# Kernel optimization log

Measured on AMD Instinct MI355X. Metric: run time of the kernel, lower is better.

## Reference

```python
import jax, jax.numpy as jnp
import numpy as np

def setup_inputs() -> dict:
    key = jax.random.key(0)
    k1, k2, k3, k4 = jax.random.split(key, 4)
    B, T, C, H = 4, 4096, 1024, 64
    x = jax.random.normal(k1, (B, T, C), dtype=jnp.float32)
    Wk = jax.random.normal(k2, (C, H), dtype=jnp.float32) * (C ** -0.5)
    Wq = jax.random.normal(k3, (C, H), dtype=jnp.float32) * (C ** -0.5)
    Wv = jax.random.normal(k4, (C, H), dtype=jnp.float32) * (C ** -0.5)
    return {"x": x, "Wk": Wk, "Wq": Wq, "Wv": Wv}

def reference(x, Wk, Wq, Wv):
    B, T, C = x.shape
    k = x @ Wk          # [B,T,H]
    q = x @ Wq          # [B,T,H]
    v = x @ Wv          # [B,T,H]
    # NOTE: original scales by C**-0.5 (full embed dim), not head_size**-0.5
    scale = C ** -0.5
    wei = jnp.einsum('bqh,bkh->bqk', q, k) * scale          # [B,T,T]
    causal = jnp.tril(jnp.ones((T, T), dtype=bool))
    wei = jnp.where(causal, wei, -jnp.inf)
    wei = jax.nn.softmax(wei, axis=-1)
    # dropout is identity in eval mode
    out = jnp.einsum('bqk,bkh->bqh', wei, v)                # [B,T,H]
    return out
```

## Files before the change

kernel.cpp:

```cpp
#include <hip/hip_runtime.h>
#include <hip/hip_bf16.h>
#include <stdint.h>

#define T_SEQ 4096
#define CDIM 1024
#define HDIM 64
#define M0 4.0f

typedef __attribute__((ext_vector_type(8))) short short8;
typedef __attribute__((ext_vector_type(4))) short short4v;
typedef __attribute__((ext_vector_type(8))) __bf16 bf16x8;
typedef __attribute__((ext_vector_type(4))) float f32x4;

static __device__ __forceinline__ short f2bf(float f) {
    uint32_t u = __builtin_bit_cast(uint32_t, f);
    u += 0x7FFFu + ((u >> 16) & 1u);
    return (short)(u >> 16);
}

static __device__ __forceinline__ f32x4 mfma16(short8 a, short8 b, f32x4 c) {
    return __builtin_amdgcn_mfma_f32_16x16x32_bf16(
        __builtin_bit_cast(bf16x8, a), __builtin_bit_cast(bf16x8, b), c, 0, 0, 0);
}

static __device__ __forceinline__ void gload_lds16(const void* g, void* l) {
    __builtin_amdgcn_global_load_lds(
        (const __attribute__((address_space(1))) void*)g,
        (__attribute__((address_space(3))) void*)l, 16, 0, 0);
}

__global__ void prep_w2(const float* __restrict__ Wk, const float* __restrict__ Wq,
                        const float* __restrict__ Wv, short* __restrict__ W2) {
    const int d = blockIdx.x * 256 + threadIdx.x;
    const int j = d & 7, l = (d >> 3) & 63;
    const int f = d >> 9;
    const int nt2 = f % 12, rest = f / 12;
    const int i = rest & 15, s = rest >> 4;
    const int n = s * 96 + (nt2 >> 1) * 16 + (l & 15);
    const int k = i * 64 + (nt2 & 1) * 32 + ((l >> 4) << 3) + j;
    float v;
    if (n < 64)       v = Wq[k * 64 + n] * (0.03125f * 1.44269504088896340736f);
    else if (n < 128) v = Wk[k * 64 + (n - 64)];
    else              v = Wv[k * 64 + (n - 128)];
    W2[d] = f2bf(v);
}

__global__ __launch_bounds__(256) void proj(const float* __restrict__ x,
                                            const short* __restrict__ W2,
                                            short* __restrict__ Qo,
                                            short* __restrict__ Ko,
                                            short* __restrict__ VT) {
    __shared__ __align__(16) short tX[2][2048];
    const int tid = threadIdx.x;
    const int lane = tid & 63, wave = tid >> 6;
    const int r = lane & 15, g = lane >> 4;
    const int msub = wave >> 1, nsplit = wave & 1;
    const int m0 = blockIdx.x * 32;

    const int srow = tid >> 3, sc = tid & 7;
    const float* xgp = x + (size_t)(m0 + srow) * CDIM + sc * 8;
    short* xd = &tX[0][srow * 64 + ((sc ^ (srow & 7)) << 3)];
    const int bufstride = 2048;

    const int arow = msub * 16 + r;
    const int aoff0 = arow * 64 + (((0 + g) ^ (arow & 7)) << 3);
    const int aoff1 = arow * 64 + (((4 + g) ^ (arow & 7)) << 3);

    const short* w2base = W2 + (size_t)nsplit * 16 * 6144 + lane * 8;

    f32x4 acc[6];
    #pragma unroll
    for (int i = 0; i < 6; ++i) acc[i] = (f32x4){0.f, 0.f, 0.f, 0.f};

    short8 wA[12], wB[12];
    {
        const short* wp = w2base;
        #pragma unroll
        for (int f = 0; f < 12; ++f) wA[f] = *(const short8*)(wp + f * 512);
    }

    f32x4 a0 = *(const f32x4*)(xgp);
    f32x4 a1 = *(const f32x4*)(xgp + 4);
    {
        short8 v;
        #pragma unroll
        for (int q = 0; q < 4; ++q) { v[q] = f2bf(a0[q]); v[4 + q] = f2bf(a1[q]); }
        *(short8*)xd = v;
    }
    a0 = *(const f32x4*)(xgp + 64);
    a1 = *(const f32x4*)(xgp + 64 + 4);
    __syncthreads();

    auto step = [&](int i, short8 (&WC)[12], short8 (&WN)[12]) {
        if (i + 1 < 16) {
            const short* wp = w2base + (size_t)(i + 1) * 6144;
            #pragma unroll
            for (int f = 0; f < 12; ++f) WN[f] = *(const short8*)(wp + f * 512);
        }
        if (i + 1 < 16) {
            short8 v;
            #pragma unroll
            for (int q = 0; q < 4; ++q) { v[q] = f2bf(a0[q]); v[4 + q] = f2bf(a1[q]); }
            *(short8*)(xd + ((i & 1) ? 0 : bufstride)) = v;
        }
        if (i + 2 < 16) {
            a0 = *(const f32x4*)(xgp + (i + 2) * 64);
            a1 = *(const f32x4*)(xgp + (i + 2) * 64 + 4);
        }
        const short* Xt = &tX[i & 1][0];
        short8 xf0 = *(const short8*)(Xt + aoff0);
        short8 xf1 = *(const short8*)(Xt + aoff1);
        #pragma unroll
        for (int nt = 0; nt < 6; ++nt) {
            if (nsplit == 1 && nt >= 2) {
                acc[nt] = mfma16(WC[2 * nt], xf0, acc[nt]);
                acc[nt] = mfma16(WC[2 * nt + 1], xf1, acc[nt]);
            } else {
                acc[nt] = mfma16(xf0, WC[2 * nt], acc[nt]);
                acc[nt] = mfma16(xf1, WC[2 * nt + 1], acc[nt]);
            }
        }
        __syncthreads();
    };

    for (int ii = 0; ii < 16; ii += 2) {
        step(ii, wA, wB);
        step(ii + 1, wB, wA);
    }

    const int b = m0 >> 12;
    const int tb = m0 & (T_SEQ - 1);
    if (nsplit == 0) {
        #pragma unroll
        for (int nt = 0; nt < 4; ++nt)
            #pragma unroll
            for (int rr = 0; rr < 4; ++rr)
                Qo[(size_t)(m0 + msub * 16 + g * 4 + rr) * HDIM + nt * 16 + r] = f2bf(acc[nt][rr]);
        #pragma unroll
        for (int nt = 4; nt < 6; ++nt)
            #pragma unroll
            for (int rr = 0; rr < 4; ++rr)
                Ko[(size_t)(m0 + msub * 16 + g * 4 + rr) * HDIM + (nt - 4) * 16 + r] = f2bf(acc[nt][rr]);
    } else {
        #pragma unroll
        for (int nt = 0; nt < 2; ++nt)
            #pragma unroll
            for (int rr = 0; rr < 4; ++rr)
                Ko[(size_t)(m0 + msub * 16 + g * 4 + rr) * HDIM + 32 + nt * 16 + r] = f2bf(acc[nt][rr]);
        const int kpanel = tb >> 6;
        const int kk0 = (tb & 63) + msub * 16;
        #pragma unroll
        for (int nt = 2; nt < 6; ++nt)
            #pragma unroll
            for (int rr = 0; rr < 4; ++rr) {
                const int h = (nt - 2) * 16 + g * 4 + rr;
                VT[(((size_t)b * 64 + kpanel) * 64 + h) * 64 + kk0 + r] = f2bf(acc[nt][rr]);
            }
    }
}

__global__ __launch_bounds__(256) void attn(const short* __restrict__ Q,
                                            const short* __restrict__ K,
                                            const short* __restrict__ VT,
                                            float* __restrict__ out,
                                            float* __restrict__ opart,
                                            float* __restrict__ lpart) {
    __shared__ __align__(16) short tK[2][4096];
    __shared__ __align__(16) short tV[2][4096];

    const int tid = threadIdx.x;
    const int lane = tid & 63, wave = tid >> 6;
    const int r = lane & 15, g = lane >> 4;
    const int b = blockIdx.x & 3;
    const int s = (int)(blockIdx.x >> 2) & 3;
    const int u = (int)(blockIdx.x >> 4);
    const int quad = u >> 4, v5 = u & 15;
    int qt;
    if (quad == 0)      qt = 63 - v5;
    else if (quad == 1) qt = v5;
    else if (quad == 2) qt = 47 - v5;
    else                qt = 16 + v5;
    const int qs = qt * 64 + wave * 16;
    const int n64 = qt + 1;
    const int niters = (n64 > s) ? ((n64 - s + 3) >> 2) : 0;

    const short* Qb = Q + (size_t)b * T_SEQ * HDIM;
    const short* Kb = K + (size_t)b * T_SEQ * HDIM;
    const short* Vb = VT + (size_t)b * 64 * 64 * 64;

    short8 qf0 = *(const short8*)(Qb + (qs + r) * HDIM + g * 8);
    short8 qf1 = *(const short8*)(Qb + (qs + r) * HDIM + 32 + g * 8);

    const int lrow = lane >> 3;
    const int lchk = (lane & 7) ^ lrow;
    const short* kgp0 = Kb + (size_t)(s * 64 + wave * 16 + lrow) * 64 + lchk * 8;
    const short* kgp1 = Kb + (size_t)(s * 64 + wave * 16 + 8 + lrow) * 64 + lchk * 8;
    const short* vgp0 = Vb + (size_t)s * 4096 + (wave * 16 + lrow) * 64 + lchk * 8;
    const short* vgp1 = Vb + (size_t)s * 4096 + (wave * 16 + 8 + lrow) * 64 + lchk * 8;
    const int ldso0 = (wave * 2) * 512, ldso1 = (wave * 2 + 1) * 512;

    int kfo0[4], kfo1[4];
    #pragma unroll
    for (int kk = 0; kk < 4; ++kk) {
        kfo0[kk] = (kk * 16 + r) * 64 + (((0 + g) ^ (r & 7)) << 3);
        kfo1[kk] = (kk * 16 + r) * 64 + (((4 + g) ^ (r & 7)) << 3);
    }
    int voL[2][4], voH[2][4];
    #pragma unroll
    for (int w2 = 0; w2 < 2; ++w2)
        #pragma unroll
        for (int ht = 0; ht < 4; ++ht) {
            const int h = ht * 16 + r;
            voL[w2][ht] = h * 64 + (((w2 * 4 + (g >> 1)) ^ (r & 7)) << 3) + (g & 1) * 4;
            voH[w2][ht] = h * 64 + (((w2 * 4 + 2 + (g >> 1)) ^ (r & 7)) << 3) + (g & 1) * 4;
        }

    float lrun = 0.f;
    f32x4 o[4];
    #pragma unroll
    for (int i = 0; i < 4; ++i) o[i] = (f32x4){0.f, 0.f, 0.f, 0.f};
    const int tq = qs + r;

    if (niters > 0) {
        gload_lds16(kgp0, &tK[0][ldso0]);
        gload_lds16(kgp1, &tK[0][ldso1]);
        gload_lds16(vgp0, &tV[0][ldso0]);
        gload_lds16(vgp1, &tV[0][ldso1]);
        __syncthreads();

        for (int i = 0; i < niters; ++i) {
            if (i + 1 < niters) {
                const int bn = (i + 1) & 1;
                const size_t adv = (size_t)(i + 1) * 16384;
                gload_lds16(kgp0 + adv, &tK[bn][ldso0]);
                gload_lds16(kgp1 + adv, &tK[bn][ldso1]);
                gload_lds16(vgp0 + adv, &tV[bn][ldso0]);
                gload_lds16(vgp1 + adv, &tV[bn][ldso1]);
            }
            const int ktm = (4 * i + s) * 64;
            const short* Kt = &tK[i & 1][0];
            const short* Vt = &tV[i & 1][0];

            short8 pf[2];
            __builtin_amdgcn_s_setprio(1);
            #pragma unroll
            for (int kk = 0; kk < 4; ++kk) {
                short8 kf0 = *(const short8*)(Kt + kfo0[kk]);
                short8 kf1 = *(const short8*)(Kt + kfo1[kk]);
                f32x4 sv4 = mfma16(kf0, qf0, (f32x4){0.f, 0.f, 0.f, 0.f});
                sv4 = mfma16(kf1, qf1, sv4);
                #pragma unroll
                for (int rr = 0; rr < 4; ++rr) {
                    const int kg = ktm + kk * 16 + g * 4 + rr;
                    float sv = sv4[rr];
                    sv = (kg <= tq) ? sv : -1e30f;
                    const float pv = __builtin_amdgcn_exp2f(sv - M0);
                    lrun += pv;
                    pf[kk >> 1][(kk & 1) * 4 + rr] = f2bf(pv);
                }
            }
            #pragma unroll
            for (int ht = 0; ht < 4; ++ht) {
                #pragma unroll
                for (int w2 = 0; w2 < 2; ++w2) {
                    short4v lo = *(const short4v*)(Vt + voL[w2][ht]);
                    short4v hi = *(const short4v*)(Vt + voH[w2][ht]);
                    short8 vf;
                    #pragma unroll
                    for (int q4 = 0; q4 < 4; ++q4) { vf[q4] = lo[q4]; vf[4 + q4] = hi[q4]; }
                    o[ht] = mfma16(vf, pf[w2], o[ht]);
                }
            }
            __builtin_amdgcn_s_setprio(0);
            __syncthreads();
        }
    }

    lrun += __shfl_xor(lrun, 16);
    lrun += __shfl_xor(lrun, 32);
    const int row = (b << 12) + qs + r;
    if (g == 0) lpart[s * 16384 + row] = lrun;
    float* ob = (s == 0 ? out : opart + (size_t)(s - 1) * 16384 * HDIM) + (size_t)row * HDIM;
    #pragma unroll
    for (int ht = 0; ht < 4; ++ht)
        *(f32x4*)(ob + ht * 16 + g * 4) = o[ht];
}

__global__ __launch_bounds__(256) void norm4(float* __restrict__ out,
                                             const float* __restrict__ opart,
                                             const float* __restrict__ lpart) {
    const int i4 = blockIdx.x * 256 + threadIdx.x;
    const int row = i4 >> 4;
    f32x4 v = *(const f32x4*)(out + (size_t)i4 * 4);
    #pragma unroll
    for (int s = 0; s < 3; ++s)
        v += *(const f32x4*)(opart + (size_t)s * 16384 * HDIM + (size_t)i4 * 4);
    const float inv = 1.0f / (lpart[row] + lpart[16384 + row] +
                              lpart[2 * 16384 + row] + lpart[3 * 16384 + row]);
    v *= inv;
    *(f32x4*)(out + (size_t)i4 * 4) = v;
}

extern "C" void kernel_launch(void* const* d_in, const int* in_sizes, int n_in,
                              void* d_out, int out_size, void* d_ws, size_t ws_size,
                              hipStream_t stream) {
    const float* x  = (const float*)d_in[0];
    const float* Wk = (const float*)d_in[1];
    const float* Wq = (const float*)d_in[2];
    const float* Wv = (const float*)d_in[3];
    float* out = (float*)d_out;

    char* ws = (char*)d_ws;
    short* W2 = (short*)ws;
    short* Qb = (short*)(ws + 393216);
    short* Kb = (short*)(ws + 393216 + 2097152);
    short* VT = (short*)(ws + 393216 + 2 * 2097152);
    float* opart = (float*)(ws + 393216 + 3 * 2097152);
    float* lpart = (float*)(ws + 393216 + 3 * 2097152 + 3 * 4194304);

    prep_w2<<<768, 256, 0, stream>>>(Wk, Wq, Wv, W2);
    proj<<<512, 256, 0, stream>>>(x, W2, Qb, Kb, VT);
    attn<<<1024, 256, 0, stream>>>(Qb, Kb, VT, out, opart, lpart);
    norm4<<<1024, 256, 0, stream>>>(out, opart, lpart);
}
```

Measured before the change: 56.58 us.

## Split each attention key tile across two waves per query sub-block

Doubles the attention block to 512 threads (8 waves). Each pair of waves shares one 16-row query slice, and each wave of the pair handles half of the 64-key tile. The two partial outputs and row sums are combined through shared memory at the end. This cuts the per-wave serial MFMA/exp chain per iteration in half and spreads the tile loads over more waves, which should improve latency hiding. The cost is an extra LDS reduction, a block-wide barrier, and more threads per block competing for occupancy.

```diff
diff --git a/kernel.cpp b/kernel.cpp
--- a/kernel.cpp
+++ b/kernel.cpp
@@ -159,18 +159,18 @@
     }
 }
 
-__global__ __launch_bounds__(256) void attn(const short* __restrict__ Q,
-                                            const short* __restrict__ K,
-                                            const short* __restrict__ VT,
-                                            float* __restrict__ out,
-                                            float* __restrict__ opart,
-                                            float* __restrict__ lpart) {
-    __shared__ __align__(16) short tK[2][4096];
-    __shared__ __align__(16) short tV[2][4096];
+__global__ __launch_bounds__(512, 8) void attn(const short* __restrict__ Q,
+                                               const short* __restrict__ K,
+                                               const short* __restrict__ VT,
+                                               float* __restrict__ out,
+                                               float* __restrict__ opart,
+                                               float* __restrict__ lpart) {
+    __shared__ __align__(16) short smem[16384];
 
     const int tid = threadIdx.x;
     const int lane = tid & 63, wave = tid >> 6;
     const int r = lane & 15, g = lane >> 4;
+    const int qsub = wave >> 1, kpar = wave & 1;
     const int b = blockIdx.x & 3;
     const int s = (int)(blockIdx.x >> 2) & 3;
     const int u = (int)(blockIdx.x >> 4);
@@ -180,7 +180,7 @@
     else if (quad == 1) qt = v5;
     else if (quad == 2) qt = 47 - v5;
     else                qt = 16 + v5;
-    const int qs = qt * 64 + wave * 16;
+    const int qs = qt * 64 + qsub * 16;
     const int n64 = qt + 1;
     const int niters = (n64 > s) ? ((n64 - s + 3) >> 2) : 0;
 
@@ -193,27 +193,24 @@
 
     const int lrow = lane >> 3;
     const int lchk = (lane & 7) ^ lrow;
-    const short* kgp0 = Kb + (size_t)(s * 64 + wave * 16 + lrow) * 64 + lchk * 8;
-    const short* kgp1 = Kb + (size_t)(s * 64 + wave * 16 + 8 + lrow) * 64 + lchk * 8;
-    const short* vgp0 = Vb + (size_t)s * 4096 + (wave * 16 + lrow) * 64 + lchk * 8;
-    const short* vgp1 = Vb + (size_t)s * 4096 + (wave * 16 + 8 + lrow) * 64 + lchk * 8;
-    const int ldso0 = (wave * 2) * 512, ldso1 = (wave * 2 + 1) * 512;
-
-    int kfo0[4], kfo1[4];
-    #pragma unroll
-    for (int kk = 0; kk < 4; ++kk) {
-        kfo0[kk] = (kk * 16 + r) * 64 + (((0 + g) ^ (r & 7)) << 3);
-        kfo1[kk] = (kk * 16 + r) * 64 + (((4 + g) ^ (r & 7)) << 3);
-    }
-    int voL[2][4], voH[2][4];
-    #pragma unroll
-    for (int w2 = 0; w2 < 2; ++w2)
-        #pragma unroll
-        for (int ht = 0; ht < 4; ++ht) {
-            const int h = ht * 16 + r;
-            voL[w2][ht] = h * 64 + (((w2 * 4 + (g >> 1)) ^ (r & 7)) << 3) + (g & 1) * 4;
-            voH[w2][ht] = h * 64 + (((w2 * 4 + 2 + (g >> 1)) ^ (r & 7)) << 3) + (g & 1) * 4;
-        }
+    const short* kgp = Kb + (size_t)(s * 64 + wave * 8 + lrow) * 64 + lchk * 8;
+    const short* vgp = Vb + (size_t)s * 4096 + (wave * 8 + lrow) * 64 + lchk * 8;
+    const int ldso = wave * 512;
+
+    int kfo0[2], kfo1[2];
+    #pragma unroll
+    for (int kk = 0; kk < 2; ++kk) {
+        const int row = kpar * 32 + kk * 16 + r;
+        kfo0[kk] = row * 64 + (((0 + g) ^ (row & 7)) << 3);
+        kfo1[kk] = row * 64 + (((4 + g) ^ (row & 7)) << 3);
+    }
+    int voL[4], voH[4];
+    #pragma unroll
+    for (int ht = 0; ht < 4; ++ht) {
+        const int h = ht * 16 + r;
+        voL[ht] = h * 64 + (((kpar * 4 + (g >> 1)) ^ (r & 7)) << 3) + (g & 1) * 4;
+        voH[ht] = h * 64 + (((kpar * 4 + 2 + (g >> 1)) ^ (r & 7)) << 3) + (g & 1) * 4;
+    }
 
     float lrun = 0.f;
     f32x4 o[4];
@@ -222,29 +219,25 @@
     const int tq = qs + r;
 
     if (niters > 0) {
-        gload_lds16(kgp0, &tK[0][ldso0]);
-        gload_lds16(kgp1, &tK[0][ldso1]);
-        gload_lds16(vgp0, &tV[0][ldso0]);
-        gload_lds16(vgp1, &tV[0][ldso1]);
+        gload_lds16(kgp, smem + ldso);
+        gload_lds16(vgp, smem + 8192 + ldso);
         __syncthreads();
 
         for (int i = 0; i < niters; ++i) {
             if (i + 1 < niters) {
                 const int bn = (i + 1) & 1;
                 const size_t adv = (size_t)(i + 1) * 16384;
-                gload_lds16(kgp0 + adv, &tK[bn][ldso0]);
-                gload_lds16(kgp1 + adv, &tK[bn][ldso1]);
-                gload_lds16(vgp0 + adv, &tV[bn][ldso0]);
-                gload_lds16(vgp1 + adv, &tV[bn][ldso1]);
-            }
-            const int ktm = (4 * i + s) * 64;
-            const short* Kt = &tK[i & 1][0];
-            const short* Vt = &tV[i & 1][0];
-
-            short8 pf[2];
+                gload_lds16(kgp + adv, smem + bn * 4096 + ldso);
+                gload_lds16(vgp + adv, smem + 8192 + bn * 4096 + ldso);
+            }
+            const int ktm = (4 * i + s) * 64 + kpar * 32;
+            const short* Kt = smem + (i & 1) * 4096;
+            const short* Vt = smem + 8192 + (i & 1) * 4096;
+
+            short8 pf;
             __builtin_amdgcn_s_setprio(1);
             #pragma unroll
-            for (int kk = 0; kk < 4; ++kk) {
+            for (int kk = 0; kk < 2; ++kk) {
                 short8 kf0 = *(const short8*)(Kt + kfo0[kk]);
                 short8 kf1 = *(const short8*)(Kt + kfo1[kk]);
                 f32x4 sv4 = mfma16(kf0, qf0, (f32x4){0.f, 0.f, 0.f, 0.f});
@@ -256,20 +249,17 @@
                     sv = (kg <= tq) ? sv : -1e30f;
                     const float pv = __builtin_amdgcn_exp2f(sv - M0);
                     lrun += pv;
-                    pf[kk >> 1][(kk & 1) * 4 + rr] = f2bf(pv);
+                    pf[kk * 4 + rr] = f2bf(pv);
                 }
             }
             #pragma unroll
             for (int ht = 0; ht < 4; ++ht) {
+                short4v lo = *(const short4v*)(Vt + voL[ht]);
+                short4v hi = *(const short4v*)(Vt + voH[ht]);
+                short8 vf;
                 #pragma unroll
-                for (int w2 = 0; w2 < 2; ++w2) {
-                    short4v lo = *(const short4v*)(Vt + voL[w2][ht]);
-                    short4v hi = *(const short4v*)(Vt + voH[w2][ht]);
-                    short8 vf;
-                    #pragma unroll
-                    for (int q4 = 0; q4 < 4; ++q4) { vf[q4] = lo[q4]; vf[4 + q4] = hi[q4]; }
-                    o[ht] = mfma16(vf, pf[w2], o[ht]);
-                }
+                for (int q4 = 0; q4 < 4; ++q4) { vf[q4] = lo[q4]; vf[4 + q4] = hi[q4]; }
+                o[ht] = mfma16(vf, pf, o[ht]);
             }
             __builtin_amdgcn_s_setprio(0);
             __syncthreads();
@@ -278,12 +268,26 @@
 
     lrun += __shfl_xor(lrun, 16);
     lrun += __shfl_xor(lrun, 32);
-    const int row = (b << 12) + qs + r;
-    if (g == 0) lpart[s * 16384 + row] = lrun;
-    float* ob = (s == 0 ? out : opart + (size_t)(s - 1) * 16384 * HDIM) + (size_t)row * HDIM;
-    #pragma unroll
-    for (int ht = 0; ht < 4; ++ht)
-        *(f32x4*)(ob + ht * 16 + g * 4) = o[ht];
+    float* co = (float*)smem;
+    float* cl2 = (float*)(smem + 8704);
+    if (kpar == 1) {
+        #pragma unroll
+        for (int ht = 0; ht < 4; ++ht)
+            *(f32x4*)&co[(qsub * 16 + r) * 68 + ht * 16 + g * 4] = o[ht];
+        if (g == 0) cl2[qsub * 16 + r] = lrun;
+    }
+    __syncthreads();
+    if (kpar == 0) {
+        const float L = lrun + cl2[qsub * 16 + r];
+        const int row = (b << 12) + qs + r;
+        if (g == 0) lpart[s * 16384 + row] = L;
+        float* ob = (s == 0 ? out : opart + (size_t)(s - 1) * 16384 * HDIM) + (size_t)row * HDIM;
+        #pragma unroll
+        for (int ht = 0; ht < 4; ++ht) {
+            f32x4 res = o[ht] + *(const f32x4*)&co[(qsub * 16 + r) * 68 + ht * 16 + g * 4];
+            *(f32x4*)(ob + ht * 16 + g * 4) = res;
+        }
+    }
 }
 
 __global__ __launch_bounds__(256) void norm4(float* __restrict__ out,
@@ -320,6 +324,6 @@
 
     prep_w2<<<768, 256, 0, stream>>>(Wk, Wq, Wv, W2);
     proj<<<512, 256, 0, stream>>>(x, W2, Qb, Kb, VT);
-    attn<<<1024, 256, 0, stream>>>(Qb, Kb, VT, out, opart, lpart);
+    attn<<<1024, 512, 0, stream>>>(Qb, Kb, VT, out, opart, lpart);
     norm4<<<1024, 256, 0, stream>>>(out, opart, lpart);
 }
```

Result: faster. 55.19 us (-2.4%).
